# Kernel optimization log

Measured on AMD Instinct MI355X. Metric: run time of the kernel, lower is better.

The kernel has to match this reference:

```python
import jax, jax.numpy as jnp
import numpy as np

# loss weights (module defaults)
LCLASS, LNOOBJ, LOBJ, LBOX = 1.0, 10.0, 1.0, 10.0


def setup_inputs() -> dict:
    key = jax.random.key(0)
    k1, k2, k3, k4 = jax.random.split(key, 4)
    B, A, S, D, N, NCLS = 32, 3, 52, 85, 20, 80  # D = 5 + NCLS
    X = jax.random.normal(k1, (B, A, S, S, D), dtype=jnp.float32)
    # normalized box centers/sizes in (0,1)
    yboxes = jax.random.uniform(k2, (B, N, 4), dtype=jnp.float32, minval=1e-3, maxval=0.999)
    ylabels = jax.random.randint(k3, (B, N), 0, NCLS).astype(jnp.int32)
    anchors = jax.random.uniform(k4, (A, 2), dtype=jnp.float32, minval=0.05, maxval=1.0)
    return {"X": X, "yboxes": yboxes, "ylabels": ylabels, "anchors": anchors, "nclasses": NCLS}


def reference(X, yboxes, ylabels, anchors, nclasses):
    # Faithful to the torch module: hgrid = X.shape[-3], wgrid = X.shape[-4].
    B, A = X.shape[0], anchors.shape[0]
    hgrid = X.shape[-3]
    wgrid = X.shape[-4]  # == A for X laid out [B, A, S, S, D] (original code's quirk)
    N = yboxes.shape[1]
    K = B * N

    boxes = yboxes.reshape(K, 4)           # [K,4] (x, y, w, h)
    labs = ylabels.reshape(K)              # [K]
    img = jnp.repeat(jnp.arange(B, dtype=jnp.int32), N)  # image index per box

    y = jnp.floor(boxes[:, 1] * hgrid).astype(jnp.int32)
    x = jnp.floor(boxes[:, 0] * wgrid).astype(jnp.int32)

    # `taken` is shared across the whole batch and a box claims ALL free anchors
    # at its cell (no break in the anchor loop). Hence only the globally-first
    # box hitting a cell contributes, with all A anchors.
    cell = y * wgrid + x                   # [K]
    order = jnp.arange(K, dtype=jnp.int32)
    BIG = jnp.int32(2 ** 30)
    first = jnp.full((hgrid * wgrid,), BIG, dtype=jnp.int32).at[cell].min(order)
    contrib = (first[cell] == order).astype(X.dtype)  # [K] 1.0 if this box contributes

    # Gather predictions for all anchors at each box's cell: [K, A, D]
    P = X[img, :, y, x, :]

    # objectness: BCEWithLogits vs target 1.0 -> softplus(-z)
    obj = jax.nn.softplus(-P[:, :, 0])     # [K, A]

    xrel = boxes[:, 0] * wgrid - x.astype(X.dtype)   # fractional cell offset
    yrel = boxes[:, 1] * hgrid - y.astype(X.dtype)
    w_c = boxes[:, 2][:, None] / anchors[None, :, 0]  # [K, A]
    h_c = boxes[:, 3][:, None] / anchors[None, :, 1]
    tgt = jnp.stack([
        jnp.broadcast_to(xrel[:, None], (K, A)),
        jnp.broadcast_to(yrel[:, None], (K, A)),
        w_c,
        h_c,
    ], axis=-1)                                        # [K, A, 4]
    boxl = jnp.mean((P[:, :, 1:5] - tgt) ** 2, axis=-1)  # MSE mean over 4 elems

    # classification: CE with one-hot target == -log_softmax[label]
    logp = jax.nn.log_softmax(P[:, :, 5:], axis=-1)    # [K, A, nclasses]
    idx = jnp.broadcast_to(labs[:, None, None], (K, A, 1)).astype(jnp.int32)
    clsl = -jnp.take_along_axis(logp, idx, axis=-1)[..., 0]  # [K, A]

    per = LOBJ * obj + LBOX * boxl + LCLASS * clsl     # [K, A]
    loss = jnp.sum(per.sum(axis=1) * contrib)
    return loss.reshape(1)
```

## Files before the change

kernel.cpp:

```cpp
#include <hip/hip_runtime.h>
#include <math.h>

#define BB    32
#define AA    3
#define SS    52
#define DD    85
#define NN    20
#define NCLS  80
#define KK    (BB * NN)
#define WGRID 3
#define HGRID 52
#define HW    (HGRID * WGRID)
#define BIGV  (1 << 30)

__global__ void yolo_first_kernel(const float* __restrict__ yboxes,
                                  int* __restrict__ first,
                                  float* __restrict__ out) {
    int tid = threadIdx.x;
    if (tid == 0) out[0] = 0.0f;
    for (int i = tid; i < HW; i += blockDim.x) first[i] = BIGV;
    __syncthreads();
    for (int k = tid; k < KK; k += blockDim.x) {
        float bx = yboxes[4 * k + 0];
        float by = yboxes[4 * k + 1];
        int x = (int)floorf(bx * (float)WGRID);
        int y = (int)floorf(by * (float)HGRID);
        atomicMin(&first[y * WGRID + x], k);
    }
}

__global__ void yolo_loss_kernel(const float* __restrict__ X,
                                 const float* __restrict__ yboxes,
                                 const int* __restrict__ ylabels,
                                 const float* __restrict__ anchors,
                                 const int* __restrict__ first,
                                 float* __restrict__ out) {
    int t = blockIdx.x * blockDim.x + threadIdx.x;
    float per = 0.0f;
    if (t < KK * AA) {
        int k = t / AA;
        int a = t - k * AA;
        float bx = yboxes[4 * k + 0];
        float by = yboxes[4 * k + 1];
        int x = (int)floorf(bx * (float)WGRID);
        int y = (int)floorf(by * (float)HGRID);
        if (first[y * WGRID + x] == k) {
            float bw = yboxes[4 * k + 2];
            float bh = yboxes[4 * k + 3];
            int img = k / NN;
            const float* __restrict__ P =
                X + ((((size_t)img * AA + a) * SS + y) * SS + x) * DD;

            float p[DD];
#pragma unroll
            for (int d = 0; d < DD; ++d) p[d] = P[d];

            float z = -p[0];
            float obj = fmaxf(z, 0.0f) + log1pf(expf(-fabsf(z)));

            float xrel = bx * (float)WGRID - (float)x;
            float yrel = by * (float)HGRID - (float)y;
            float wc = bw / anchors[2 * a + 0];
            float hc = bh / anchors[2 * a + 1];
            float d1 = p[1] - xrel, d2 = p[2] - yrel;
            float d3 = p[3] - wc,   d4 = p[4] - hc;
            float boxl = 0.25f * (d1 * d1 + d2 * d2 + d3 * d3 + d4 * d4);

            float m = -INFINITY;
#pragma unroll
            for (int c = 0; c < NCLS; ++c) m = fmaxf(m, p[5 + c]);
            float ssum = 0.0f;
#pragma unroll
            for (int c = 0; c < NCLS; ++c) ssum += expf(p[5 + c] - m);
            int lab = ylabels[k];
            float plab = P[5 + lab];
            float clsl = -(plab - m - logf(ssum));

            per = 1.0f * obj + 10.0f * boxl + 1.0f * clsl;
        }
    }

    __shared__ float sdata[4];
    int lane = threadIdx.x & 63;
    int wave = threadIdx.x >> 6;
    float v = per;
#pragma unroll
    for (int off = 32; off > 0; off >>= 1) v += __shfl_down(v, off, 64);
    if (lane == 0) sdata[wave] = v;
    __syncthreads();
    if (wave == 0) {
        float w = (lane < 4) ? sdata[lane] : 0.0f;
#pragma unroll
        for (int off = 32; off > 0; off >>= 1) w += __shfl_down(w, off, 64);
        if (lane == 0) atomicAdd(out, w);
    }
}

extern "C" void kernel_launch(void* const* d_in, const int* in_sizes, int n_in,
                              void* d_out, int out_size, void* d_ws, size_t ws_size,
                              hipStream_t stream) {
    const float* X       = (const float*)d_in[0];
    const float* yboxes  = (const float*)d_in[1];
    const int*   ylabels = (const int*)d_in[2];
    const float* anchors = (const float*)d_in[3];

    float* out  = (float*)d_out;
    int*   first = (int*)d_ws;

    yolo_first_kernel<<<1, 256, 0, stream>>>(yboxes, first, out);

    int tasks  = KK * AA;
    int blocks = (tasks + 255) / 256;
    yolo_loss_kernel<<<blocks, 256, 0, stream>>>(X, yboxes, ylabels, anchors,
                                                 first, out);
}
```

Measured before the change: 17.34 us.

## Fuse first-box and loss kernels into a single-block kernel with shared-memory table

Merges the two launches into one 1024-thread block. The first-box table now lives in shared memory, and the final sum is written directly instead of through a global atomic. This removes a kernel launch, the global workspace round trip and the zero-initialisation dependency. In exchange, all 1920 tasks run on a single CU, so gathering the 85-float rows is serialized over two iterations per thread with less memory parallelism.

```diff
diff --git a/kernel.cpp b/kernel.cpp
--- a/kernel.cpp
+++ b/kernel.cpp
@@ -12,87 +12,85 @@
 #define HGRID 52
 #define HW    (HGRID * WGRID)
 #define BIGV  (1 << 30)
+#define NTHREADS 1024
 
-__global__ void yolo_first_kernel(const float* __restrict__ yboxes,
-                                  int* __restrict__ first,
-                                  float* __restrict__ out) {
-    int tid = threadIdx.x;
-    if (tid == 0) out[0] = 0.0f;
-    for (int i = tid; i < HW; i += blockDim.x) first[i] = BIGV;
+__global__ void __launch_bounds__(NTHREADS)
+yolo_fused_kernel(const float* __restrict__ X,
+                  const float* __restrict__ yboxes,
+                  const int* __restrict__ ylabels,
+                  const float* __restrict__ anchors,
+                  float* __restrict__ out) {
+    __shared__ int   first[HW];
+    __shared__ float sdata[NTHREADS / 64];
+
+    const int tid = threadIdx.x;
+
+    if (tid < HW) first[tid] = BIGV;
     __syncthreads();
-    for (int k = tid; k < KK; k += blockDim.x) {
-        float bx = yboxes[4 * k + 0];
-        float by = yboxes[4 * k + 1];
+    if (tid < KK) {
+        float bx = yboxes[4 * tid + 0];
+        float by = yboxes[4 * tid + 1];
         int x = (int)floorf(bx * (float)WGRID);
         int y = (int)floorf(by * (float)HGRID);
-        atomicMin(&first[y * WGRID + x], k);
+        atomicMin(&first[y * WGRID + x], tid);
     }
-}
+    __syncthreads();
 
-__global__ void yolo_loss_kernel(const float* __restrict__ X,
-                                 const float* __restrict__ yboxes,
-                                 const int* __restrict__ ylabels,
-                                 const float* __restrict__ anchors,
-                                 const int* __restrict__ first,
-                                 float* __restrict__ out) {
-    int t = blockIdx.x * blockDim.x + threadIdx.x;
-    float per = 0.0f;
-    if (t < KK * AA) {
+    float acc = 0.0f;
+    for (int t = tid; t < KK * AA; t += NTHREADS) {
         int k = t / AA;
         int a = t - k * AA;
         float bx = yboxes[4 * k + 0];
         float by = yboxes[4 * k + 1];
         int x = (int)floorf(bx * (float)WGRID);
         int y = (int)floorf(by * (float)HGRID);
-        if (first[y * WGRID + x] == k) {
-            float bw = yboxes[4 * k + 2];
-            float bh = yboxes[4 * k + 3];
-            int img = k / NN;
-            const float* __restrict__ P =
-                X + ((((size_t)img * AA + a) * SS + y) * SS + x) * DD;
+        if (first[y * WGRID + x] != k) continue;
 
-            float p[DD];
+        float bw = yboxes[4 * k + 2];
+        float bh = yboxes[4 * k + 3];
+        int img = k / NN;
+        const float* __restrict__ P =
+            X + ((((size_t)img * AA + a) * SS + y) * SS + x) * DD;
+
+        float p[DD];
 #pragma unroll
-            for (int d = 0; d < DD; ++d) p[d] = P[d];
+        for (int d = 0; d < DD; ++d) p[d] = P[d];
 
-            float z = -p[0];
-            float obj = fmaxf(z, 0.0f) + log1pf(expf(-fabsf(z)));
+        float z = -p[0];
+        float obj = fmaxf(z, 0.0f) + log1pf(expf(-fabsf(z)));
 
-            float xrel = bx * (float)WGRID - (float)x;
-            float yrel = by * (float)HGRID - (float)y;
-            float wc = bw / anchors[2 * a + 0];
-            float hc = bh / anchors[2 * a + 1];
-            float d1 = p[1] - xrel, d2 = p[2] - yrel;
-            float d3 = p[3] - wc,   d4 = p[4] - hc;
-            float boxl = 0.25f * (d1 * d1 + d2 * d2 + d3 * d3 + d4 * d4);
+        float xrel = bx * (float)WGRID - (float)x;
+        float yrel = by * (float)HGRID - (float)y;
+        float wc = bw / anchors[2 * a + 0];
+        float hc = bh / anchors[2 * a + 1];
+        float d1 = p[1] - xrel, d2 = p[2] - yrel;
+        float d3 = p[3] - wc,   d4 = p[4] - hc;
+        float boxl = 0.25f * (d1 * d1 + d2 * d2 + d3 * d3 + d4 * d4);
 
-            float m = -INFINITY;
+        float m = -INFINITY;
 #pragma unroll
-            for (int c = 0; c < NCLS; ++c) m = fmaxf(m, p[5 + c]);
-            float ssum = 0.0f;
+        for (int c = 0; c < NCLS; ++c) m = fmaxf(m, p[5 + c]);
+        float ssum = 0.0f;
 #pragma unroll
-            for (int c = 0; c < NCLS; ++c) ssum += expf(p[5 + c] - m);
-            int lab = ylabels[k];
-            float plab = P[5 + lab];
-            float clsl = -(plab - m - logf(ssum));
+        for (int c = 0; c < NCLS; ++c) ssum += expf(p[5 + c] - m);
+        int lab = ylabels[k];
+        float plab = P[5 + lab];
+        float clsl = -(plab - m - logf(ssum));
 
-            per = 1.0f * obj + 10.0f * boxl + 1.0f * clsl;
-        }
+        acc += 1.0f * obj + 10.0f * boxl + 1.0f * clsl;
     }
 
-    __shared__ float sdata[4];
-    int lane = threadIdx.x & 63;
-    int wave = threadIdx.x >> 6;
-    float v = per;
+    const int lane = tid & 63;
+    const int wave = tid >> 6;
 #pragma unroll
-    for (int off = 32; off > 0; off >>= 1) v += __shfl_down(v, off, 64);
-    if (lane == 0) sdata[wave] = v;
+    for (int off = 32; off > 0; off >>= 1) acc += __shfl_down(acc, off, 64);
+    if (lane == 0) sdata[wave] = acc;
     __syncthreads();
     if (wave == 0) {
-        float w = (lane < 4) ? sdata[lane] : 0.0f;
+        float w = (lane < NTHREADS / 64) ? sdata[lane] : 0.0f;
 #pragma unroll
         for (int off = 32; off > 0; off >>= 1) w += __shfl_down(w, off, 64);
-        if (lane == 0) atomicAdd(out, w);
+        if (lane == 0) out[0] = w;
     }
 }
 
@@ -104,13 +102,8 @@
     const int*   ylabels = (const int*)d_in[2];
     const float* anchors = (const float*)d_in[3];
 
-    float* out  = (float*)d_out;
-    int*   first = (int*)d_ws;
+    float* out = (float*)d_out;
 
-    yolo_first_kernel<<<1, 256, 0, stream>>>(yboxes, first, out);
-
-    int tasks  = KK * AA;
-    int blocks = (tasks + 255) / 256;
-    yolo_loss_kernel<<<blocks, 256, 0, stream>>>(X, yboxes, ylabels, anchors,
-                                                 first, out);
+    yolo_fused_kernel<<<1, NTHREADS, 0, stream>>>(X, yboxes, ylabels, anchors,
+                                                  out);
 }
```

Result: slower. 22.42 us (+29.3%).
